# Optimization experiments

Measured on AMD Instinct MI355X. Metric: run time of the kernel, lower is better.

## Reference

```python
import jax, jax.numpy as jnp
import numpy as np

EPS = 1e-12

def squash(s):
    # standard capsule squash: ||s||^2/(1+||s||^2) * s/||s||
    n2 = jnp.sum(s * s, axis=-1, keepdims=True)
    return n2 / (1.0 + n2) * s / jnp.sqrt(n2 + EPS)

def setup_inputs() -> dict:
    key = jax.random.key(0)
    k1, k2 = jax.random.split(key)
    B, O, I, DOUT, DIN = 64, 32, 2048, 16, 16
    u = jax.random.normal(k1, (B, I, DIN), dtype=jnp.float32)
    # TruncatedNormal(stddev=0.1) init for W
    W = 0.1 * jax.random.truncated_normal(k2, -2.0, 2.0, (1, O, I, DOUT, DIN), dtype=jnp.float32)
    bias = jnp.full((1, O, DOUT), 0.1, dtype=jnp.float32)
    return {"u": u, "W": W, "bias": bias}

def reference(u, W, bias):
    routing_iterations = 3
    O = W.shape[1]
    # u: [B, I, DIN], W: [1, O, I, DOUT, DIN]
    u_norm = jnp.linalg.norm(u, axis=-1)                     # [B, I]
    # u_hat[b,o,i,d] = sum_k W[0,o,i,d,k] * u[b,i,k]  (batched matmul instead of tile+mul+sum)
    u_hat = jnp.einsum('oidk,bik->boid', W[0], u)            # [B, O, I, DOUT]
    u_hat_norm = jnp.linalg.norm(u_hat, axis=-1, keepdims=True)   # [B, O, I, 1]
    new_u_hat_norm = jnp.minimum(u_hat_norm, u_norm[:, None, :, None])
    u_hat = u_hat / (u_hat_norm + EPS) * new_u_hat_norm

    B = u.shape[0]
    b_ij = jnp.zeros((B, O, u.shape[1], 1), dtype=u.dtype)
    t_const = jnp.float32(np.log(0.9 * (O - 1)) - np.log(1.0 - 0.9))
    v_j = None
    c_ij = None
    for r in range(routing_iterations):
        c_ij = jax.nn.softmax(b_ij, axis=1)                  # softmax over out capsules
        s_j = jnp.sum(c_ij * u_hat, axis=2) + bias           # [B, O, DOUT]
        v_j = squash(s_j)
        if r < routing_iterations - 1:
            # gamma-routing agreement: distance between prediction and output
            d = jnp.linalg.norm(v_j[:, :, None, :] - u_hat, axis=-1, keepdims=True)  # [B,O,I,1]
            d_o = jnp.mean(d)
            d_p = d_o * 0.5
            t = t_const / (d_p - d_o + 1e-12)
            b_ij = t * d
    return (v_j, c_ij)
```

## Files before the change

### kernel.cpp

```cpp
#include <hip/hip_runtime.h>
#include <hip/hip_bf16.h>
#include <math.h>

#define BB 64
#define OO 32
#define II 2048
#define DD 16
#define CAPS_EPS 1e-12f
#define T_CONST 5.6312118f

#define GX 128
#define TI 16

#define OFF_DSUM 0ULL
#define OFF_V     16ULL
#define OFF_UNORM 32784ULL
#define OFF_UBF   163856ULL
#define OFF_WB    1212432ULL
#define OFF_DD    9601040ULL
#define OFF_CB    13795344ULL
#define OFF_PART  17989648ULL
#define OFF_SCALE 22183952ULL
#define OFF_NN2   26378256ULL

typedef __attribute__((ext_vector_type(8))) short bf16x8;
typedef __attribute__((ext_vector_type(4))) float f32x4;

union AU { bf16x8 v; unsigned short h[8]; uint4 u4; };

__device__ __forceinline__ unsigned short f2bf(float x) {
    __hip_bfloat16 h = __float2bfloat16(x);
    unsigned short s; __builtin_memcpy(&s, &h, 2); return s;
}

__global__ __launch_bounds__(256) void uprep_kernel(
    const float* __restrict__ u, float* __restrict__ ws)
{
    const int gid = blockIdx.x * 256 + threadIdx.x;
    if (gid < 2) ws[OFF_DSUM + gid] = 0.f;
    const int i = gid >> 6, b = gid & 63;

    const float4* up = reinterpret_cast<const float4*>(u + ((size_t)b * II + i) * DD);
    float4 t0 = up[0], t1 = up[1], t2 = up[2], t3 = up[3];
    float un2 = t0.x*t0.x + t0.y*t0.y + t0.z*t0.z + t0.w*t0.w
              + t1.x*t1.x + t1.y*t1.y + t1.z*t1.z + t1.w*t1.w
              + t2.x*t2.x + t2.y*t2.y + t2.z*t2.z + t2.w*t2.w
              + t3.x*t3.x + t3.y*t3.y + t3.z*t3.z + t3.w*t3.w;
    ws[OFF_UNORM + (size_t)i * 64 + b] = __builtin_amdgcn_sqrtf(un2);

    AU a0, a1;
    a0.h[0]=f2bf(t0.x); a0.h[1]=f2bf(t0.y); a0.h[2]=f2bf(t0.z); a0.h[3]=f2bf(t0.w);
    a0.h[4]=f2bf(t1.x); a0.h[5]=f2bf(t1.y); a0.h[6]=f2bf(t1.z); a0.h[7]=f2bf(t1.w);
    a1.h[0]=f2bf(t2.x); a1.h[1]=f2bf(t2.y); a1.h[2]=f2bf(t2.z); a1.h[3]=f2bf(t2.w);
    a1.h[4]=f2bf(t3.x); a1.h[5]=f2bf(t3.y); a1.h[6]=f2bf(t3.z); a1.h[7]=f2bf(t3.w);
    unsigned short* ubf = (unsigned short*)(ws + OFF_UBF);
    uint4* dst = reinterpret_cast<uint4*>(ubf + ((size_t)i * 64 + b) * 16);
    dst[0] = a0.u4; dst[1] = a1.u4;
}

__global__ __launch_bounds__(256) void s0w_kernel(
    const float* __restrict__ W, float* __restrict__ ws)
{
    const int og   = blockIdx.y;
    const int wave = threadIdx.x >> 6;
    const int lane = threadIdx.x & 63;
    const int o    = og * 4 + wave;
    const int q    = lane >> 4;
    const int n    = lane & 15;

    unsigned short* Wb = (unsigned short*)(ws + OFF_WB);
    const unsigned short* ubf = (const unsigned short*)(ws + OFF_UBF);
    const float* unorm = ws + OFF_UNORM;
    float* part = ws + OFF_PART;
    float* scl  = ws + OFF_SCALE;
    float* nn2w = ws + OFF_NN2;

    f32x4 s_acc[4];
    #pragma unroll
    for (int g = 0; g < 4; ++g) s_acc[g] = (f32x4){0.f, 0.f, 0.f, 0.f};

    for (int ii = 0; ii < TI; ++ii) {
        const int i = blockIdx.x * TI + ii;

        AU au; au.u4 = make_uint4(0, 0, 0, 0);
        if (q < 2) {
            const float* wp = W + (((size_t)o * II + i) * 16 + n) * 16 + q * 8;
            float4 w0 = *(const float4*)(wp);
            float4 w1 = *(const float4*)(wp + 4);
            au.h[0]=f2bf(w0.x); au.h[1]=f2bf(w0.y); au.h[2]=f2bf(w0.z); au.h[3]=f2bf(w0.w);
            au.h[4]=f2bf(w1.x); au.h[5]=f2bf(w1.y); au.h[6]=f2bf(w1.z); au.h[7]=f2bf(w1.w);
            *reinterpret_cast<uint4*>(Wb + (((size_t)o * II + i) * 2 + q) * 128 + n * 8) = au.u4;
        }

        f32x4 d4[4];
        #pragma unroll
        for (int g = 0; g < 4; ++g) {
            AU bu;
            bu.u4 = *reinterpret_cast<const uint4*>(
                ubf + ((size_t)i * 64 + g * 16 + n) * 16 + (q & 1) * 8);
            d4[g] = __builtin_amdgcn_mfma_f32_16x16x32_bf16(
                au.v, bu.v, (f32x4){0.f, 0.f, 0.f, 0.f}, 0, 0, 0);
        }

        #pragma unroll
        for (int g = 0; g < 4; ++g) {
            float n2 = d4[g][0]*d4[g][0] + d4[g][1]*d4[g][1]
                     + d4[g][2]*d4[g][2] + d4[g][3]*d4[g][3];
            n2 += __shfl_xor(n2, 16);
            n2 += __shfl_xor(n2, 32);
            const float rsq  = __builtin_amdgcn_rsqf(n2 + CAPS_EPS);
            const float rawn = n2 * rsq;
            const float un = unorm[(size_t)i * 64 + g * 16 + n];
            const float nn = fminf(rawn, un);
            const float scale = nn * rsq;
            if (q == 0) {
                const size_t idx = ((size_t)i * OO + o) * 64 + g * 16 + n;
                scl[idx]  = scale;
                nn2w[idx] = nn * nn;
            }
            const float cs = 0.03125f * scale;
            s_acc[g][0] += cs * d4[g][0];
            s_acc[g][1] += cs * d4[g][1];
            s_acc[g][2] += cs * d4[g][2];
            s_acc[g][3] += cs * d4[g][3];
        }
    }

    #pragma unroll
    for (int g = 0; g < 4; ++g) {
        float4 v = make_float4(s_acc[g][0], s_acc[g][1], s_acc[g][2], s_acc[g][3]);
        *reinterpret_cast<float4*>(
            part + (((size_t)blockIdx.x * OO + o) * 64 + g * 16 + n) * 16 + q * 4) = v;
    }
}

template<int SLOT>
__global__ __launch_bounds__(256) void dpass_kernel(float* __restrict__ ws)
{
    const int og   = blockIdx.y >> 1;
    const int bh   = blockIdx.y & 1;
    const int wave = threadIdx.x >> 6;
    const int lane = threadIdx.x & 63;
    const int o    = og * 4 + wave;
    const int q    = lane >> 4;
    const int n    = lane & 15;

    const unsigned short* Wb  = (const unsigned short*)(ws + OFF_WB);
    const unsigned short* ubf = (const unsigned short*)(ws + OFF_UBF);
    const float* v_ws = ws + OFF_V;
    const float* scl  = ws + OFF_SCALE;
    const float* nn2w = ws + OFF_NN2;
    float* dws = ws + OFF_DD;

    f32x4 vreg[2];
    float vn2[2];
    #pragma unroll
    for (int gg = 0; gg < 2; ++gg) {
        const int g = bh * 2 + gg;
        vreg[gg] = *reinterpret_cast<const f32x4*>(
            v_ws + ((size_t)(g * 16 + n) * OO + o) * 16 + q * 4);
        float t = vreg[gg][0]*vreg[gg][0] + vreg[gg][1]*vreg[gg][1]
                + vreg[gg][2]*vreg[gg][2] + vreg[gg][3]*vreg[gg][3];
        t += __shfl_xor(t, 16);
        t += __shfl_xor(t, 32);
        vn2[gg] = t;
    }

    float dsum_local = 0.f;

    for (int ii = 0; ii < TI; ++ii) {
        const int i = blockIdx.x * TI + ii;

        AU au; au.u4 = make_uint4(0, 0, 0, 0);
        if (q < 2)
            au.u4 = *reinterpret_cast<const uint4*>(
                Wb + (((size_t)o * II + i) * 2 + q) * 128 + n * 8);

        #pragma unroll
        for (int gg = 0; gg < 2; ++gg) {
            const int g = bh * 2 + gg;
            AU bu;
            bu.u4 = *reinterpret_cast<const uint4*>(
                ubf + ((size_t)i * 64 + g * 16 + n) * 16 + (q & 1) * 8);
            f32x4 d4 = __builtin_amdgcn_mfma_f32_16x16x32_bf16(
                au.v, bu.v, (f32x4){0.f, 0.f, 0.f, 0.f}, 0, 0, 0);

            float pp = vreg[gg][0]*d4[0] + vreg[gg][1]*d4[1]
                     + vreg[gg][2]*d4[2] + vreg[gg][3]*d4[3];
            pp += __shfl_xor(pp, 16);
            pp += __shfl_xor(pp, 32);

            const size_t idx = ((size_t)i * OO + o) * 64 + g * 16 + n;
            const float sc  = scl[idx];
            const float dd2 = fmaxf(vn2[gg] + nn2w[idx] - 2.f * sc * pp, 0.f);
            const float dist = __builtin_amdgcn_sqrtf(dd2);
            if (q == 0) {
                dws[idx] = dist;
                dsum_local += dist;
            }
        }
    }

    #pragma unroll
    for (int off = 32; off > 0; off >>= 1)
        dsum_local += __shfl_down(dsum_local, off);
    __shared__ float red[4];
    if (lane == 0) red[wave] = dsum_local;
    __syncthreads();
    if (threadIdx.x == 0)
        atomicAdd(&ws[OFF_DSUM + SLOT], red[0] + red[1] + red[2] + red[3]);
}

template<int SLOT>
__global__ __launch_bounds__(256) void csoft_kernel(float* __restrict__ ws)
{
    const int wave = threadIdx.x >> 6;
    const int b    = threadIdx.x & 63;
    const int i    = blockIdx.x * 4 + wave;

    const float* dws = ws + OFF_DD;
    float* cb = ws + OFF_CB;
    const float dsum = ws[OFF_DSUM + SLOT];
    const float tval = T_CONST * __builtin_amdgcn_rcpf(
        -0.5f * dsum * (1.0f / 4194304.0f) + 1e-12f);

    float dv[OO];
    #pragma unroll
    for (int o = 0; o < OO; ++o)
        dv[o] = tval * dws[((size_t)i * OO + o) * 64 + b];
    float m = -1e30f;
    #pragma unroll
    for (int o = 0; o < OO; ++o) m = fmaxf(m, dv[o]);
    float ssum = 0.f;
    #pragma unroll
    for (int o = 0; o < OO; ++o) { dv[o] = __expf(dv[o] - m); ssum += dv[o]; }
    const float inv = __builtin_amdgcn_rcpf(ssum);
    #pragma unroll
    for (int o = 0; o < OO; ++o)
        cb[((size_t)i * OO + o) * 64 + b] = dv[o] * inv;
}

__global__ __launch_bounds__(256) void spass_kernel(float* __restrict__ ws)
{
    const int og   = blockIdx.y >> 1;
    const int bh   = blockIdx.y & 1;
    const int wave = threadIdx.x >> 6;
    const int lane = threadIdx.x & 63;
    const int o    = og * 4 + wave;
    const int q    = lane >> 4;
    const int n    = lane & 15;

    const unsigned short* Wb  = (const unsigned short*)(ws + OFF_WB);
    const unsigned short* ubf = (const unsigned short*)(ws + OFF_UBF);
    const float* cb  = ws + OFF_CB;
    const float* scl = ws + OFF_SCALE;
    float* part = ws + OFF_PART;

    f32x4 s_acc[2];
    #pragma unroll
    for (int gg = 0; gg < 2; ++gg) s_acc[gg] = (f32x4){0.f, 0.f, 0.f, 0.f};

    for (int ii = 0; ii < TI; ++ii) {
        const int i = blockIdx.x * TI + ii;

        AU au; au.u4 = make_uint4(0, 0, 0, 0);
        if (q < 2)
            au.u4 = *reinterpret_cast<const uint4*>(
                Wb + (((size_t)o * II + i) * 2 + q) * 128 + n * 8);

        #pragma unroll
        for (int gg = 0; gg < 2; ++gg) {
            const int g = bh * 2 + gg;
            AU bu;
            bu.u4 = *reinterpret_cast<const uint4*>(
                ubf + ((size_t)i * 64 + g * 16 + n) * 16 + (q & 1) * 8);
            f32x4 d4 = __builtin_amdgcn_mfma_f32_16x16x32_bf16(
                au.v, bu.v, (f32x4){0.f, 0.f, 0.f, 0.f}, 0, 0, 0);

            const size_t idx = ((size_t)i * OO + o) * 64 + g * 16 + n;
            const float cs = cb[idx] * scl[idx];
            s_acc[gg][0] += cs * d4[0];
            s_acc[gg][1] += cs * d4[1];
            s_acc[gg][2] += cs * d4[2];
            s_acc[gg][3] += cs * d4[3];
        }
    }

    #pragma unroll
    for (int gg = 0; gg < 2; ++gg) {
        const int g = bh * 2 + gg;
        float4 v = make_float4(s_acc[gg][0], s_acc[gg][1], s_acc[gg][2], s_acc[gg][3]);
        *reinterpret_cast<float4*>(
            part + (((size_t)blockIdx.x * OO + o) * 64 + g * 16 + n) * 16 + q * 4) = v;
    }
}

__global__ __launch_bounds__(256) void finv_kernel(
    const float* __restrict__ part, const float* __restrict__ bias,
    float* __restrict__ vout)
{
    const int tid = blockIdx.x * 256 + threadIdx.x;
    float s = 0.f;
    #pragma unroll 4
    for (int ic = 0; ic < GX; ++ic)
        s += part[(size_t)ic * (OO * 64 * 16) + (tid >> 9) * 16 + ((tid >> 4) & 31) * 1024 + (tid & 15)];
    s += bias[tid & 511];
    float n2 = s * s;
    #pragma unroll
    for (int off = 1; off < 16; off <<= 1) n2 += __shfl_xor(n2, off);
    vout[tid] = s * n2 * __builtin_amdgcn_rcpf(1.f + n2)
                  * __builtin_amdgcn_rsqf(n2 + CAPS_EPS);
}

__global__ __launch_bounds__(256) void transpose_kernel(
    const float* __restrict__ cb, float* __restrict__ dst)
{
    __shared__ float tile[32][65];
    const int o  = blockIdx.y;
    const int i0 = blockIdx.x * 32;
    #pragma unroll
    for (int k = 0; k < 8; ++k) {
        const int lin = k * 256 + threadIdx.x;
        const int r = lin >> 6, b = lin & 63;
        tile[r][b] = cb[((size_t)(i0 + r) * OO + o) * 64 + b];
    }
    __syncthreads();
    #pragma unroll
    for (int k = 0; k < 8; ++k) {
        const int lin = k * 256 + threadIdx.x;
        const int b = lin >> 5, r = lin & 31;
        dst[((size_t)b * OO + o) * II + i0 + r] = tile[r][b];
    }
}

extern "C" void kernel_launch(void* const* d_in, const int* in_sizes, int n_in,
                              void* d_out, int out_size, void* d_ws, size_t ws_size,
                              hipStream_t stream) {
    const float* u    = (const float*)d_in[0];
    const float* W    = (const float*)d_in[1];
    const float* bias = (const float*)d_in[2];
    float* out = (float*)d_out;
    float* ws  = (float*)d_ws;

    float* part = ws + OFF_PART;
    float* v_ws = ws + OFF_V;
    float* cb   = ws + OFF_CB;
    float* cout = out + (size_t)BB * OO * DD;

    dim3 blk(256);
    dim3 grid_m(GX, 8);
    dim3 grid_d(GX, 16);

    uprep_kernel<<<512, blk, 0, stream>>>(u, ws);
    s0w_kernel<<<grid_m, blk, 0, stream>>>(W, ws);
    finv_kernel<<<128, blk, 0, stream>>>(part, bias, v_ws);
    dpass_kernel<0><<<grid_d, blk, 0, stream>>>(ws);
    csoft_kernel<0><<<512, blk, 0, stream>>>(ws);
    spass_kernel<<<grid_d, blk, 0, stream>>>(ws);
    finv_kernel<<<128, blk, 0, stream>>>(part, bias, v_ws);
    dpass_kernel<1><<<grid_d, blk, 0, stream>>>(ws);
    csoft_kernel<1><<<512, blk, 0, stream>>>(ws);
    spass_kernel<<<grid_d, blk, 0, stream>>>(ws);
    finv_kernel<<<128, blk, 0, stream>>>(part, bias, out);
    transpose_kernel<<<dim3(64, 32), blk, 0, stream>>>(cb, cout);
}
```

Baseline: 353.2 us.

## Materialize scaled u_hat in fp16 and drop MFMA recompute in routing passes

The first pass now stores the clipped, rescaled u_hat as fp16 (64 MiB) instead of a bf16 copy of W plus scale/norm arrays, and the routing passes stream this tensor rather than recomputing u_hat with MFMA. Softmax coefficients are no longer materialized; only per-(i,b) max and denominator are stored and c_ij is recomputed from distances where needed. Partial-sum buffers plus a reduction pass are replaced with float atomics into per-iteration S buffers. This trades recompute and extra scalar arrays for a large fp16 read per pass, adds fp16 rounding of u_hat, and makes the sums order-nondeterministic.

```diff
diff --git a/kernel.cpp b/kernel.cpp
--- a/kernel.cpp
+++ b/kernel.cpp
@@ -1,5 +1,6 @@
 #include <hip/hip_runtime.h>
 #include <hip/hip_bf16.h>
+#include <hip/hip_fp16.h>
 #include <math.h>
 
 #define BB 64
@@ -9,24 +10,26 @@
 #define CAPS_EPS 1e-12f
 #define T_CONST 5.6312118f
 
-#define GX 128
-#define TI 16
-
-#define OFF_DSUM 0ULL
-#define OFF_V     16ULL
-#define OFF_UNORM 32784ULL
-#define OFF_UBF   163856ULL
-#define OFF_WB    1212432ULL
-#define OFF_DD    9601040ULL
-#define OFF_CB    13795344ULL
-#define OFF_PART  17989648ULL
-#define OFF_SCALE 22183952ULL
-#define OFF_NN2   26378256ULL
+#define TIS 8
+#define SLEN 16
+#define NSTRIP 128
+
+#define OFF_DSUM  0ULL
+#define OFF_S     16ULL
+#define OFF_V     98320ULL
+#define OFF_UNORM 131088ULL
+#define OFF_UBF   262160ULL
+#define OFF_Y     1310736ULL
+#define OFF_DD    34865168ULL
+#define OFF_TMAX  39059472ULL
+#define OFF_TDEN  39190544ULL
 
 typedef __attribute__((ext_vector_type(8))) short bf16x8;
 typedef __attribute__((ext_vector_type(4))) float f32x4;
 
 union AU { bf16x8 v; unsigned short h[8]; uint4 u4; };
+union YU { __half h[4]; uint2 u2; };
+union YL { uint4 u4[2]; __half h[16]; };
 
 __device__ __forceinline__ unsigned short f2bf(float x) {
     __hip_bfloat16 h = __float2bfloat16(x);
@@ -38,6 +41,7 @@
 {
     const int gid = blockIdx.x * 256 + threadIdx.x;
     if (gid < 2) ws[OFF_DSUM + gid] = 0.f;
+    if (gid < 3 * 32768) ws[OFF_S + gid] = 0.f;
     const int i = gid >> 6, b = gid & 63;
 
     const float4* up = reinterpret_cast<const float4*>(u + ((size_t)b * II + i) * DD);
@@ -68,19 +72,17 @@
     const int q    = lane >> 4;
     const int n    = lane & 15;
 
-    unsigned short* Wb = (unsigned short*)(ws + OFF_WB);
     const unsigned short* ubf = (const unsigned short*)(ws + OFF_UBF);
     const float* unorm = ws + OFF_UNORM;
-    float* part = ws + OFF_PART;
-    float* scl  = ws + OFF_SCALE;
-    float* nn2w = ws + OFF_NN2;
+    __half* Y = (__half*)(ws + OFF_Y);
+    float* S0 = ws + OFF_S;
 
     f32x4 s_acc[4];
     #pragma unroll
     for (int g = 0; g < 4; ++g) s_acc[g] = (f32x4){0.f, 0.f, 0.f, 0.f};
 
-    for (int ii = 0; ii < TI; ++ii) {
-        const int i = blockIdx.x * TI + ii;
+    for (int ii = 0; ii < TIS; ++ii) {
+        const int i = blockIdx.x * TIS + ii;
 
         AU au; au.u4 = make_uint4(0, 0, 0, 0);
         if (q < 2) {
@@ -89,7 +91,6 @@
             float4 w1 = *(const float4*)(wp + 4);
             au.h[0]=f2bf(w0.x); au.h[1]=f2bf(w0.y); au.h[2]=f2bf(w0.z); au.h[3]=f2bf(w0.w);
             au.h[4]=f2bf(w1.x); au.h[5]=f2bf(w1.y); au.h[6]=f2bf(w1.z); au.h[7]=f2bf(w1.w);
-            *reinterpret_cast<uint4*>(Wb + (((size_t)o * II + i) * 2 + q) * 128 + n * 8) = au.u4;
         }
 
         f32x4 d4[4];
@@ -111,13 +112,16 @@
             const float rsq  = __builtin_amdgcn_rsqf(n2 + CAPS_EPS);
             const float rawn = n2 * rsq;
             const float un = unorm[(size_t)i * 64 + g * 16 + n];
-            const float nn = fminf(rawn, un);
-            const float scale = nn * rsq;
-            if (q == 0) {
-                const size_t idx = ((size_t)i * OO + o) * 64 + g * 16 + n;
-                scl[idx]  = scale;
-                nn2w[idx] = nn * nn;
-            }
+            const float scale = fminf(rawn, un) * rsq;
+
+            YU yu;
+            yu.h[0] = __float2half(scale * d4[g][0]);
+            yu.h[1] = __float2half(scale * d4[g][1]);
+            yu.h[2] = __float2half(scale * d4[g][2]);
+            yu.h[3] = __float2half(scale * d4[g][3]);
+            *reinterpret_cast<uint2*>(
+                Y + (((size_t)i * OO + o) * 64 + g * 16 + n) * 16 + q * 4) = yu.u2;
+
             const float cs = 0.03125f * scale;
             s_acc[g][0] += cs * d4[g][0];
             s_acc[g][1] += cs * d4[g][1];
@@ -127,99 +131,81 @@
     }
 
     #pragma unroll
-    for (int g = 0; g < 4; ++g) {
-        float4 v = make_float4(s_acc[g][0], s_acc[g][1], s_acc[g][2], s_acc[g][3]);
-        *reinterpret_cast<float4*>(
-            part + (((size_t)blockIdx.x * OO + o) * 64 + g * 16 + n) * 16 + q * 4) = v;
-    }
+    for (int g = 0; g < 4; ++g)
+        #pragma unroll
+        for (int r = 0; r < 4; ++r)
+            atomicAdd(&S0[(((size_t)(g * 16 + n)) * OO + o) * 16 + q * 4 + r],
+                      s_acc[g][r]);
+}
+
+__global__ __launch_bounds__(256) void finv_kernel(
+    const float* __restrict__ sbuf, const float* __restrict__ bias,
+    float* __restrict__ vout)
+{
+    const int tid = blockIdx.x * 256 + threadIdx.x;
+    float s = sbuf[tid] + bias[tid & 511];
+    float n2 = s * s;
+    #pragma unroll
+    for (int off = 1; off < 16; off <<= 1) n2 += __shfl_xor(n2, off);
+    vout[tid] = s * n2 * __builtin_amdgcn_rcpf(1.f + n2)
+                  * __builtin_amdgcn_rsqf(n2 + CAPS_EPS);
 }
 
 template<int SLOT>
 __global__ __launch_bounds__(256) void dpass_kernel(float* __restrict__ ws)
 {
-    const int og   = blockIdx.y >> 1;
-    const int bh   = blockIdx.y & 1;
-    const int wave = threadIdx.x >> 6;
-    const int lane = threadIdx.x & 63;
-    const int o    = og * 4 + wave;
-    const int q    = lane >> 4;
-    const int n    = lane & 15;
-
-    const unsigned short* Wb  = (const unsigned short*)(ws + OFF_WB);
-    const unsigned short* ubf = (const unsigned short*)(ws + OFF_UBF);
+    const int strip = blockIdx.x;
+    const int og    = blockIdx.y;
+    const int wave  = threadIdx.x >> 6;
+    const int b     = threadIdx.x & 63;
+    const int o     = og * 4 + wave;
+
+    const __half* Y   = (const __half*)(ws + OFF_Y);
     const float* v_ws = ws + OFF_V;
-    const float* scl  = ws + OFF_SCALE;
-    const float* nn2w = ws + OFF_NN2;
     float* dws = ws + OFF_DD;
 
-    f32x4 vreg[2];
-    float vn2[2];
-    #pragma unroll
-    for (int gg = 0; gg < 2; ++gg) {
-        const int g = bh * 2 + gg;
-        vreg[gg] = *reinterpret_cast<const f32x4*>(
-            v_ws + ((size_t)(g * 16 + n) * OO + o) * 16 + q * 4);
-        float t = vreg[gg][0]*vreg[gg][0] + vreg[gg][1]*vreg[gg][1]
-                + vreg[gg][2]*vreg[gg][2] + vreg[gg][3]*vreg[gg][3];
-        t += __shfl_xor(t, 16);
-        t += __shfl_xor(t, 32);
-        vn2[gg] = t;
-    }
-
-    float dsum_local = 0.f;
-
-    for (int ii = 0; ii < TI; ++ii) {
-        const int i = blockIdx.x * TI + ii;
-
-        AU au; au.u4 = make_uint4(0, 0, 0, 0);
-        if (q < 2)
-            au.u4 = *reinterpret_cast<const uint4*>(
-                Wb + (((size_t)o * II + i) * 2 + q) * 128 + n * 8);
-
-        #pragma unroll
-        for (int gg = 0; gg < 2; ++gg) {
-            const int g = bh * 2 + gg;
-            AU bu;
-            bu.u4 = *reinterpret_cast<const uint4*>(
-                ubf + ((size_t)i * 64 + g * 16 + n) * 16 + (q & 1) * 8);
-            f32x4 d4 = __builtin_amdgcn_mfma_f32_16x16x32_bf16(
-                au.v, bu.v, (f32x4){0.f, 0.f, 0.f, 0.f}, 0, 0, 0);
-
-            float pp = vreg[gg][0]*d4[0] + vreg[gg][1]*d4[1]
-                     + vreg[gg][2]*d4[2] + vreg[gg][3]*d4[3];
-            pp += __shfl_xor(pp, 16);
-            pp += __shfl_xor(pp, 32);
-
-            const size_t idx = ((size_t)i * OO + o) * 64 + g * 16 + n;
-            const float sc  = scl[idx];
-            const float dd2 = fmaxf(vn2[gg] + nn2w[idx] - 2.f * sc * pp, 0.f);
-            const float dist = __builtin_amdgcn_sqrtf(dd2);
-            if (q == 0) {
-                dws[idx] = dist;
-                dsum_local += dist;
-            }
+    float v[16];
+    float vn2 = 0.f;
+    #pragma unroll
+    for (int k = 0; k < 16; ++k) {
+        v[k] = v_ws[((size_t)b * OO + o) * 16 + k];
+        vn2 += v[k] * v[k];
+    }
+
+    float acc = 0.f;
+    #pragma unroll 4
+    for (int s = 0; s < SLEN; ++s) {
+        const int i = strip * SLEN + s;
+        const uint4* yp = reinterpret_cast<const uint4*>(
+            Y + (((size_t)i * OO + o) * 64 + b) * 16);
+        YL yl;
+        yl.u4[0] = yp[0];
+        yl.u4[1] = yp[1];
+        float dot = 0.f, yn2 = 0.f;
+        #pragma unroll
+        for (int k = 0; k < 16; ++k) {
+            const float y = __half2float(yl.h[k]);
+            dot += v[k] * y;
+            yn2 += y * y;
         }
-    }
-
-    #pragma unroll
-    for (int off = 32; off > 0; off >>= 1)
-        dsum_local += __shfl_down(dsum_local, off);
-    __shared__ float red[4];
-    if (lane == 0) red[wave] = dsum_local;
-    __syncthreads();
-    if (threadIdx.x == 0)
-        atomicAdd(&ws[OFF_DSUM + SLOT], red[0] + red[1] + red[2] + red[3]);
+        const float dd2 = fmaxf(vn2 - 2.f * dot + yn2, 0.f);
+        const float dist = __builtin_amdgcn_sqrtf(dd2);
+        dws[((size_t)i * OO + o) * 64 + b] = dist;
+        acc += dist;
+    }
+
+    #pragma unroll
+    for (int off = 32; off > 0; off >>= 1) acc += __shfl_down(acc, off);
+    if ((threadIdx.x & 63) == 0) atomicAdd(&ws[OFF_DSUM + SLOT], acc);
 }
 
 template<int SLOT>
 __global__ __launch_bounds__(256) void csoft_kernel(float* __restrict__ ws)
 {
-    const int wave = threadIdx.x >> 6;
-    const int b    = threadIdx.x & 63;
-    const int i    = blockIdx.x * 4 + wave;
+    const int gid = blockIdx.x * 256 + threadIdx.x;
+    const int i = gid >> 6, b = gid & 63;
 
     const float* dws = ws + OFF_DD;
-    float* cb = ws + OFF_CB;
     const float dsum = ws[OFF_DSUM + SLOT];
     const float tval = T_CONST * __builtin_amdgcn_rcpf(
         -0.5f * dsum * (1.0f / 4194304.0f) + 1e-12f);
@@ -231,98 +217,79 @@
     float m = -1e30f;
     #pragma unroll
     for (int o = 0; o < OO; ++o) m = fmaxf(m, dv[o]);
-    float ssum = 0.f;
-    #pragma unroll
-    for (int o = 0; o < OO; ++o) { dv[o] = __expf(dv[o] - m); ssum += dv[o]; }
-    const float inv = __builtin_amdgcn_rcpf(ssum);
-    #pragma unroll
-    for (int o = 0; o < OO; ++o)
-        cb[((size_t)i * OO + o) * 64 + b] = dv[o] * inv;
-}
-
+    float den = 0.f;
+    #pragma unroll
+    for (int o = 0; o < OO; ++o) den += __expf(dv[o] - m);
+    ws[OFF_TMAX + (size_t)i * 64 + b] = m;
+    ws[OFF_TDEN + (size_t)i * 64 + b] = den;
+}
+
+template<int SLOT, int SIDX>
 __global__ __launch_bounds__(256) void spass_kernel(float* __restrict__ ws)
 {
-    const int og   = blockIdx.y >> 1;
-    const int bh   = blockIdx.y & 1;
-    const int wave = threadIdx.x >> 6;
-    const int lane = threadIdx.x & 63;
-    const int o    = og * 4 + wave;
-    const int q    = lane >> 4;
-    const int n    = lane & 15;
-
-    const unsigned short* Wb  = (const unsigned short*)(ws + OFF_WB);
-    const unsigned short* ubf = (const unsigned short*)(ws + OFF_UBF);
-    const float* cb  = ws + OFF_CB;
-    const float* scl = ws + OFF_SCALE;
-    float* part = ws + OFF_PART;
-
-    f32x4 s_acc[2];
-    #pragma unroll
-    for (int gg = 0; gg < 2; ++gg) s_acc[gg] = (f32x4){0.f, 0.f, 0.f, 0.f};
-
-    for (int ii = 0; ii < TI; ++ii) {
-        const int i = blockIdx.x * TI + ii;
-
-        AU au; au.u4 = make_uint4(0, 0, 0, 0);
-        if (q < 2)
-            au.u4 = *reinterpret_cast<const uint4*>(
-                Wb + (((size_t)o * II + i) * 2 + q) * 128 + n * 8);
-
-        #pragma unroll
-        for (int gg = 0; gg < 2; ++gg) {
-            const int g = bh * 2 + gg;
-            AU bu;
-            bu.u4 = *reinterpret_cast<const uint4*>(
-                ubf + ((size_t)i * 64 + g * 16 + n) * 16 + (q & 1) * 8);
-            f32x4 d4 = __builtin_amdgcn_mfma_f32_16x16x32_bf16(
-                au.v, bu.v, (f32x4){0.f, 0.f, 0.f, 0.f}, 0, 0, 0);
-
-            const size_t idx = ((size_t)i * OO + o) * 64 + g * 16 + n;
-            const float cs = cb[idx] * scl[idx];
-            s_acc[gg][0] += cs * d4[0];
-            s_acc[gg][1] += cs * d4[1];
-            s_acc[gg][2] += cs * d4[2];
-            s_acc[gg][3] += cs * d4[3];
-        }
-    }
-
-    #pragma unroll
-    for (int gg = 0; gg < 2; ++gg) {
-        const int g = bh * 2 + gg;
-        float4 v = make_float4(s_acc[gg][0], s_acc[gg][1], s_acc[gg][2], s_acc[gg][3]);
-        *reinterpret_cast<float4*>(
-            part + (((size_t)blockIdx.x * OO + o) * 64 + g * 16 + n) * 16 + q * 4) = v;
-    }
-}
-
-__global__ __launch_bounds__(256) void finv_kernel(
-    const float* __restrict__ part, const float* __restrict__ bias,
-    float* __restrict__ vout)
-{
-    const int tid = blockIdx.x * 256 + threadIdx.x;
-    float s = 0.f;
+    const int strip = blockIdx.x;
+    const int og    = blockIdx.y;
+    const int wave  = threadIdx.x >> 6;
+    const int b     = threadIdx.x & 63;
+    const int o     = og * 4 + wave;
+
+    const __half* Y = (const __half*)(ws + OFF_Y);
+    const float* dws  = ws + OFF_DD;
+    const float* tmax = ws + OFF_TMAX;
+    const float* tden = ws + OFF_TDEN;
+    float* S = ws + OFF_S + (size_t)SIDX * 32768;
+
+    const float dsum = ws[OFF_DSUM + SLOT];
+    const float tval = T_CONST * __builtin_amdgcn_rcpf(
+        -0.5f * dsum * (1.0f / 4194304.0f) + 1e-12f);
+
+    float acc[16];
+    #pragma unroll
+    for (int k = 0; k < 16; ++k) acc[k] = 0.f;
+
     #pragma unroll 4
-    for (int ic = 0; ic < GX; ++ic)
-        s += part[(size_t)ic * (OO * 64 * 16) + (tid >> 9) * 16 + ((tid >> 4) & 31) * 1024 + (tid & 15)];
-    s += bias[tid & 511];
-    float n2 = s * s;
-    #pragma unroll
-    for (int off = 1; off < 16; off <<= 1) n2 += __shfl_xor(n2, off);
-    vout[tid] = s * n2 * __builtin_amdgcn_rcpf(1.f + n2)
-                  * __builtin_amdgcn_rsqf(n2 + CAPS_EPS);
+    for (int s = 0; s < SLEN; ++s) {
+        const int i = strip * SLEN + s;
+        const uint4* yp = reinterpret_cast<const uint4*>(
+            Y + (((size_t)i * OO + o) * 64 + b) * 16);
+        YL yl;
+        yl.u4[0] = yp[0];
+        yl.u4[1] = yp[1];
+        const float d  = dws[((size_t)i * OO + o) * 64 + b];
+        const float m  = tmax[(size_t)i * 64 + b];
+        const float dn = tden[(size_t)i * 64 + b];
+        const float p = __expf(tval * d - m) * __builtin_amdgcn_rcpf(dn);
+        #pragma unroll
+        for (int k = 0; k < 16; ++k)
+            acc[k] += p * __half2float(yl.h[k]);
+    }
+
+    #pragma unroll
+    for (int k = 0; k < 16; ++k)
+        atomicAdd(&S[((size_t)b * OO + o) * 16 + k], acc[k]);
 }
 
 __global__ __launch_bounds__(256) void transpose_kernel(
-    const float* __restrict__ cb, float* __restrict__ dst)
+    const float* __restrict__ ws, float* __restrict__ dst)
 {
     __shared__ float tile[32][65];
+    const float* dws  = ws + OFF_DD;
+    const float* tmax = ws + OFF_TMAX;
+    const float* tden = ws + OFF_TDEN;
+    const float dsum = ws[OFF_DSUM + 1];
+    const float tval = T_CONST * __builtin_amdgcn_rcpf(
+        -0.5f * dsum * (1.0f / 4194304.0f) + 1e-12f);
+
     const int o  = blockIdx.y;
     const int i0 = blockIdx.x * 32;
     #pragma unroll
     for (int k = 0; k < 8; ++k) {
         const int lin = k * 256 + threadIdx.x;
         const int r = lin >> 6, b = lin & 63;
-        tile[r][b] = cb[((size_t)(i0 + r) * OO + o) * 64 + b];
+        const int i = i0 + r;
+        const float d = dws[((size_t)i * OO + o) * 64 + b];
+        tile[r][b] = __expf(tval * d - tmax[(size_t)i * 64 + b])
+                   * __builtin_amdgcn_rcpf(tden[(size_t)i * 64 + b]);
     }
     __syncthreads();
     #pragma unroll
@@ -342,25 +309,23 @@
     float* out = (float*)d_out;
     float* ws  = (float*)d_ws;
 
-    float* part = ws + OFF_PART;
     float* v_ws = ws + OFF_V;
-    float* cb   = ws + OFF_CB;
     float* cout = out + (size_t)BB * OO * DD;
 
     dim3 blk(256);
-    dim3 grid_m(GX, 8);
-    dim3 grid_d(GX, 16);
+    dim3 grid_w(256, 8);
+    dim3 grid_s(NSTRIP, 8);
 
     uprep_kernel<<<512, blk, 0, stream>>>(u, ws);
-    s0w_kernel<<<grid_m, blk, 0, stream>>>(W, ws);
-    finv_kernel<<<128, blk, 0, stream>>>(part, bias, v_ws);
-    dpass_kernel<0><<<grid_d, blk, 0, stream>>>(ws);
+    s0w_kernel<<<grid_w, blk, 0, stream>>>(W, ws);
+    finv_kernel<<<128, blk, 0, stream>>>(ws + OFF_S, bias, v_ws);
+    dpass_kernel<0><<<grid_s, blk, 0, stream>>>(ws);
     csoft_kernel<0><<<512, blk, 0, stream>>>(ws);
-    spass_kernel<<<grid_d, blk, 0, stream>>>(ws);
-    finv_kernel<<<128, blk, 0, stream>>>(part, bias, v_ws);
-    dpass_kernel<1><<<grid_d, blk, 0, stream>>>(ws);
+    spass_kernel<0, 1><<<grid_s, blk, 0, stream>>>(ws);
+    finv_kernel<<<128, blk, 0, stream>>>(ws + OFF_S + 32768, bias, v_ws);
+    dpass_kernel<1><<<grid_s, blk, 0, stream>>>(ws);
     csoft_kernel<1><<<512, blk, 0, stream>>>(ws);
-    spass_kernel<<<grid_d, blk, 0, stream>>>(ws);
-    finv_kernel<<<128, blk, 0, stream>>>(part, bias, out);
-    transpose_kernel<<<dim3(64, 32), blk, 0, stream>>>(cb, cout);
-}
+    spass_kernel<1, 2><<<grid_s, blk, 0, stream>>>(ws);
+    finv_kernel<<<128, blk, 0, stream>>>(ws + OFF_S + 65536, bias, out);
+    transpose_kernel<<<dim3(64, 32), blk, 0, stream>>>(ws, cout);
+}
```

After: 1.203 ms. 3.41x slower.
